# Kernel tuning notes

Hardware: AMD Instinct MI355X
Metric: run time of the kernel (lower is better)

Reference implementation:

```python
import jax, jax.numpy as jnp
import numpy as np

DIM = 384
HEADS = 8
RATES = (0.5, 0.75)  # sparse_rates
EPS = 1e-12  # torch F.normalize default eps


def _dwconv3x3(x, w):
    # depthwise 3x3, padding=1; w: [3*dim, 1, 3, 3]
    return jax.lax.conv_general_dilated(
        x, w, window_strides=(1, 1), padding=((1, 1), (1, 1)),
        feature_group_count=w.shape[0],
        dimension_numbers=('NCHW', 'OIHW', 'NCHW'))


def setup_inputs() -> dict:
    key = jax.random.key(0)
    ks = jax.random.split(key, 5)
    dim = DIM
    x = jax.random.normal(ks[0], (4, dim, 128, 128), jnp.float32)
    qkv_w = jax.random.normal(ks[1], (3 * dim, dim), jnp.float32) * 0.05   # 1x1 conv
    dw_w = jax.random.normal(ks[2], (3 * dim, 1, 3, 3), jnp.float32) * 0.1  # depthwise 3x3
    proj_w = jax.random.normal(ks[3], (dim, dim), jnp.float32) * 0.05       # 1x1 conv
    temperature = jnp.ones((HEADS, 1, 1), jnp.float32)
    attns = jnp.full((len(RATES),), 0.2, jnp.float32)
    return {"x": x, "qkv_w": qkv_w, "dw_w": dw_w, "proj_w": proj_w,
            "temperature": temperature, "attns": attns}


def reference(x, qkv_w, dw_w, proj_w, temperature, attns) -> jnp.ndarray:
    b, c, h, w = x.shape
    qkv = jnp.einsum('bchw,oc->bohw', x, qkv_w)  # 1x1 conv, no bias
    qkv = _dwconv3x3(qkv, dw_w)
    q, k, v = jnp.split(qkv, 3, axis=1)

    def heads(t):  # b (head c) h w -> b head c (h w)
        return t.reshape(b, HEADS, c // HEADS, h * w)

    q, k, v = heads(q), heads(k), heads(v)
    q = q / jnp.maximum(jnp.linalg.norm(q, axis=-1, keepdims=True), EPS)
    k = k / jnp.maximum(jnp.linalg.norm(k, axis=-1, keepdims=True), EPS)
    C = q.shape[2]
    attn = jnp.einsum('bhcn,bhdn->bhcd', q, k) * temperature  # [b, head, C, C]

    out = jnp.zeros_like(v)  # [b, head, C, HW]
    for i, rate in enumerate(RATES):
        kk = int(C * rate)
        _, idx = jax.lax.top_k(attn, kk)                      # [b, head, C, kk]
        mask = jax.nn.one_hot(idx, C, dtype=attn.dtype).sum(-2) > 0  # scatter 1s
        attn = jnp.where(mask, attn, -jnp.inf)
        attn = jax.nn.softmax(attn, axis=-1)  # NOTE: original reuses softmaxed attn next iter
        out = out + jnp.einsum('bhcd,bhdn->bhcn', attn, v) * attns[i]

    out = out.reshape(b, c, h, w)  # b head c (hw) -> b (head c) h w
    return jnp.einsum('bchw,oc->bohw', out, proj_w)
```

## Files before the change

### kernel.cpp

```cpp
#include <hip/hip_runtime.h>
#include <math.h>

#define HW     16384
#define WIDTH  128
#define CDIM   384
#define QKVC   1152
#define HEADS  8
#define CH     48
#define NSPLIT 32
#define GK     384

typedef unsigned short u16;
typedef short bf16x8 __attribute__((ext_vector_type(8)));
typedef u16 u16x8 __attribute__((ext_vector_type(8)));
typedef float f32x4 __attribute__((ext_vector_type(4)));

__device__ __forceinline__ void split2(float x, u16& h, u16& l) {
    union { float f; unsigned u; } a, b, c;
    a.f = x;
    unsigned hu = (a.u + 0x7fffu + ((a.u >> 16) & 1u)) & 0xffff0000u;
    b.u = hu;
    h = (u16)(hu >> 16);
    c.f = x - b.f;
    l = (u16)((c.u + 0x7fffu + ((c.u >> 16) & 1u)) >> 16);
}

__device__ __forceinline__ void gload16(const void* g, void* l) {
    __builtin_amdgcn_global_load_lds((const __attribute__((address_space(1))) unsigned int*)g,
                                     (__attribute__((address_space(3))) unsigned int*)l, 16, 0, 0);
}

__global__ __launch_bounds__(256)
void mfma_gemm(const u16* __restrict__ Ah, const u16* __restrict__ Al,
               const u16* __restrict__ Bh, const u16* __restrict__ Bl,
               float* __restrict__ C, int nmb,
               long abs_, long bbs, long cbs)
{
    extern __shared__ char smem[];
    const int tot = gridDim.x * gridDim.y;
    const int per = tot >> 3;
    const int fl  = blockIdx.x + gridDim.x * blockIdx.y;
    const int f2  = (fl & 7) * per + (fl >> 3);
    const int nblk = f2 / nmb, mblk = f2 % nmb;
    const int b = blockIdx.z;
    Ah += (long)b * abs_; Al += (long)b * abs_;
    Bh += (long)b * bbs;  Bl += (long)b * bbs;
    C  += (long)b * cbs;
    const int m0 = mblk * 128, n0 = nblk * 128;

    const int tid  = threadIdx.x;
    const int wave = tid >> 6, lane = tid & 63;
    const int lr = lane & 15, lg = lane >> 4;
    const int wm = wave >> 1, wn = wave & 1;

    const int srow = tid >> 2;
    const int kc   = tid & 3;
    const int sw   = kc ^ ((srow >> 1) & 3);

    f32x4 acc[4][4];
#pragma unroll
    for (int i = 0; i < 4; ++i)
#pragma unroll
        for (int j = 0; j < 4; ++j) acc[i][j] = (f32x4){0.f, 0.f, 0.f, 0.f};

#define STAGE(bs, kt) do { char* LL = smem + (bs) * 32768;                          \
        const long ko = (long)(kt) * 32 + sw * 8;                                   \
        gload16(Ah + (long)(m0 + srow) * GK      + ko, LL + tid * 16);              \
        gload16(Ah + (long)(m0 + 64 + srow) * GK + ko, LL + 4096  + tid * 16);      \
        gload16(Al + (long)(m0 + srow) * GK      + ko, LL + 8192  + tid * 16);      \
        gload16(Al + (long)(m0 + 64 + srow) * GK + ko, LL + 12288 + tid * 16);      \
        gload16(Bh + (long)(n0 + srow) * GK      + ko, LL + 16384 + tid * 16);      \
        gload16(Bh + (long)(n0 + 64 + srow) * GK + ko, LL + 20480 + tid * 16);      \
        gload16(Bl + (long)(n0 + srow) * GK      + ko, LL + 24576 + tid * 16);      \
        gload16(Bl + (long)(n0 + 64 + srow) * GK + ko, LL + 28672 + tid * 16);      \
    } while (0)

    STAGE(0, 0);
    __syncthreads();
#pragma unroll
    for (int kt = 0; kt < 12; ++kt) {
        if (kt + 1 < 12) STAGE((kt + 1) & 1, kt + 1);

        const char* L = smem + (kt & 1) * 32768;
        bf16x8 af[4][2], bf[4][2];
#pragma unroll
        for (int mi = 0; mi < 4; ++mi) {
            int r = wm * 64 + mi * 16 + lr;
            int off = r * 64 + (((lg ^ (r >> 1)) & 3) << 4);
            af[mi][0] = *(const bf16x8*)(L + off);
            af[mi][1] = *(const bf16x8*)(L + 8192 + off);
        }
#pragma unroll
        for (int ni = 0; ni < 4; ++ni) {
            int r = wn * 64 + ni * 16 + lr;
            int off = r * 64 + (((lg ^ (r >> 1)) & 3) << 4);
            bf[ni][0] = *(const bf16x8*)(L + 16384 + off);
            bf[ni][1] = *(const bf16x8*)(L + 24576 + off);
        }

        __builtin_amdgcn_s_setprio(1);
#pragma unroll
        for (int mi = 0; mi < 4; ++mi)
#pragma unroll
            for (int ni = 0; ni < 4; ++ni) {
                acc[mi][ni] = __builtin_amdgcn_mfma_f32_16x16x32_bf16(af[mi][0], bf[ni][0], acc[mi][ni], 0, 0, 0);
                acc[mi][ni] = __builtin_amdgcn_mfma_f32_16x16x32_bf16(af[mi][0], bf[ni][1], acc[mi][ni], 0, 0, 0);
                acc[mi][ni] = __builtin_amdgcn_mfma_f32_16x16x32_bf16(af[mi][1], bf[ni][0], acc[mi][ni], 0, 0, 0);
            }
        __builtin_amdgcn_s_setprio(0);
        __syncthreads();
    }
#undef STAGE

#pragma unroll
    for (int mi = 0; mi < 4; ++mi)
#pragma unroll
        for (int ni = 0; ni < 4; ++ni) {
            int row = m0 + wm * 64 + mi * 16 + lg * 4;
            int col = n0 + wn * 64 + ni * 16 + lr;
            float* cp = C + (long)row * HW + col;
            cp[0]          = acc[mi][ni][0];
            cp[(long)HW]   = acc[mi][ni][1];
            cp[2L * HW]    = acc[mi][ni][2];
            cp[3L * HW]    = acc[mi][ni][3];
        }
}

__global__ __launch_bounds__(256)
void convT_kernel(const float* __restrict__ in, u16* __restrict__ oh, u16* __restrict__ ol,
                  long ibs, long obs)
{
    const int b = blockIdx.z;
    in += (long)b * ibs; oh += (long)b * obs; ol += (long)b * obs;
    __shared__ float t[32][33];
    const int p0 = blockIdx.x * 32, c0 = blockIdx.y * 32;
    const int ty = threadIdx.x >> 5, tx = threadIdx.x & 31;
#pragma unroll
    for (int it = 0; it < 4; ++it) {
        int c = ty + it * 8;
        t[c][tx] = in[(long)(c0 + c) * HW + p0 + tx];
    }
    __syncthreads();
    const int cp = threadIdx.x & 15;
    const int py = threadIdx.x >> 4;
#pragma unroll
    for (int half = 0; half < 2; ++half) {
        int p = py + half * 16;
        u16 h0, l0, h1, l1;
        split2(t[2 * cp][p], h0, l0);
        split2(t[2 * cp + 1][p], h1, l1);
        long o = (long)(p0 + p) * CDIM + c0 + 2 * cp;
        *(ushort2*)&oh[o] = (ushort2){h0, h1};
        *(ushort2*)&ol[o] = (ushort2){l0, l1};
    }
}

__global__ __launch_bounds__(256)
void convA_kernel(const float* __restrict__ in, u16* __restrict__ oh, u16* __restrict__ ol, int n)
{
    int i = blockIdx.x * 256 + threadIdx.x;
    if (i < n) split2(in[i], oh[i], ol[i]);
}

__global__ __launch_bounds__(256)
void dwconv_kernel(const float* __restrict__ in, const float* __restrict__ w,
                   float* __restrict__ out)
{
    const long base = (long)blockIdx.y * QKVC * HW;
    const int idx = blockIdx.x * 256 + threadIdx.x;
    const int ch = idx >> 11;
    const int wi = idx & 2047;
    const int y = wi >> 4, x0 = (wi & 15) * 8;
    const float* wp = w + ch * 9;
    const float* ip = in + base + (long)ch * HW;
    float o[8] = {0.f, 0.f, 0.f, 0.f, 0.f, 0.f, 0.f, 0.f};
#pragma unroll
    for (int dy = -1; dy <= 1; ++dy) {
        int yy = y + dy;
        if ((unsigned)yy >= 128u) continue;
        const float* rp = ip + yy * WIDTH + x0;
        float4 a  = *(const float4*)rp;
        float4 bq = *(const float4*)(rp + 4);
        float v[10] = { (x0 > 0) ? rp[-1] : 0.f,
                        a.x, a.y, a.z, a.w, bq.x, bq.y, bq.z, bq.w,
                        (x0 < 120) ? rp[8] : 0.f };
        float w0 = wp[(dy + 1) * 3], w1 = wp[(dy + 1) * 3 + 1], w2 = wp[(dy + 1) * 3 + 2];
#pragma unroll
        for (int j = 0; j < 8; ++j)
            o[j] = fmaf(w0, v[j], fmaf(w1, v[j + 1], fmaf(w2, v[j + 2], o[j])));
    }
    float* op = out + base + (long)ch * HW + y * WIDTH + x0;
    *(float4*)op       = (float4){o[0], o[1], o[2], o[3]};
    *(float4*)(op + 4) = (float4){o[4], o[5], o[6], o[7]};
}

__global__ __launch_bounds__(256)
void dwconv_vT_kernel(const float* __restrict__ in, const float* __restrict__ w,
                      u16* __restrict__ oh, u16* __restrict__ ol, long ibs, long obs)
{
    const int b  = blockIdx.z;
    const int cg = blockIdx.y;
    const int p0 = blockIdx.x * 64;
    const int y  = p0 >> 7, xh = p0 & 127;
    __shared__ unsigned pk[64][97];

    const int tid = threadIdx.x;
    const int seg = tid & 7;
    const int chl = tid >> 3;
    const int x0  = xh + seg * 8;
#pragma unroll
    for (int cp = 0; cp < 3; ++cp) {
        const int cl = cp * 32 + chl;
        const int c  = cg * 96 + cl;
        const float* ip = in + (long)b * ibs + (long)(768 + c) * HW;
        const float* wp = w + (768 + c) * 9;
        float o[8] = {0.f, 0.f, 0.f, 0.f, 0.f, 0.f, 0.f, 0.f};
#pragma unroll
        for (int dy = -1; dy <= 1; ++dy) {
            int yy = y + dy;
            if ((unsigned)yy >= 128u) continue;
            const float* rp = ip + yy * WIDTH + x0;
            float4 a  = *(const float4*)rp;
            float4 bq = *(const float4*)(rp + 4);
            float v[10] = { (x0 > 0) ? rp[-1] : 0.f,
                            a.x, a.y, a.z, a.w, bq.x, bq.y, bq.z, bq.w,
                            (x0 < 120) ? rp[8] : 0.f };
            float w0 = wp[(dy + 1) * 3], w1 = wp[(dy + 1) * 3 + 1], w2 = wp[(dy + 1) * 3 + 2];
#pragma unroll
            for (int j = 0; j < 8; ++j)
                o[j] = fmaf(w0, v[j], fmaf(w1, v[j + 1], fmaf(w2, v[j + 2], o[j])));
        }
#pragma unroll
        for (int j = 0; j < 8; ++j) {
            u16 hh, ll;
            split2(o[j], hh, ll);
            pk[seg * 8 + j][cl] = ((unsigned)hh << 16) | ll;
        }
    }
    __syncthreads();
    const int px = tid >> 2, qt = tid & 3;
    u16 hs[24], ls[24];
#pragma unroll
    for (int j = 0; j < 24; ++j) {
        unsigned v = pk[px][qt * 24 + j];
        hs[j] = (u16)(v >> 16);
        ls[j] = (u16)(v & 0xffffu);
    }
    u16* ph = oh + (long)b * obs + (long)(p0 + px) * CDIM + cg * 96 + qt * 24;
    u16* pl = ol + (long)b * obs + (long)(p0 + px) * CDIM + cg * 96 + qt * 24;
#pragma unroll
    for (int j = 0; j < 3; ++j) {
        *(u16x8*)(ph + j * 8) = *(const u16x8*)&hs[j * 8];
        *(u16x8*)(pl + j * 8) = *(const u16x8*)&ls[j * 8];
    }
}

__global__ __launch_bounds__(256)
void attn_partial_kernel(const float* __restrict__ dw, float* __restrict__ part,
                         float* __restrict__ part2, long ps, long p2s)
{
    const int split = blockIdx.x, h = blockIdx.y, b = blockIdx.z;
    const int n0 = split * (HW / NSPLIT);
    const float* qbase = dw + ((long)b * QKVC + h * CH) * HW;
    const float* kbase = dw + ((long)b * QKVC + CDIM + h * CH) * HW;
    __shared__ float qs[64][49];
    __shared__ float ks[64][49];
    const int tid = threadIdx.x;
    const int tr = tid >> 4, tc = tid & 15;
    const int c0 = tr * 3, d0 = tc * 3;
    float acc[3][3] = {{0.f}};
    float qss[3] = {0.f, 0.f, 0.f}, kss[3] = {0.f, 0.f, 0.f};
    const int cA = tid >> 4;
    const int nq = (tid & 15) * 4;
    for (int ns = 0; ns < HW / NSPLIT; ns += 64) {
        __syncthreads();
#pragma unroll
        for (int t = 0; t < 3; ++t) {
            int c = cA + t * 16;
            float4 qv = *(const float4*)(qbase + (long)c * HW + n0 + ns + nq);
            float4 kv = *(const float4*)(kbase + (long)c * HW + n0 + ns + nq);
            qs[nq + 0][c] = qv.x; qs[nq + 1][c] = qv.y;
            qs[nq + 2][c] = qv.z; qs[nq + 3][c] = qv.w;
            ks[nq + 0][c] = kv.x; ks[nq + 1][c] = kv.y;
            ks[nq + 2][c] = kv.z; ks[nq + 3][c] = kv.w;
            qss[t] += qv.x * qv.x + qv.y * qv.y + qv.z * qv.z + qv.w * qv.w;
            kss[t] += kv.x * kv.x + kv.y * kv.y + kv.z * kv.z + kv.w * kv.w;
        }
        __syncthreads();
#pragma unroll 8
        for (int n = 0; n < 64; ++n) {
            float q0 = qs[n][c0], q1 = qs[n][c0 + 1], q2 = qs[n][c0 + 2];
            float k0 = ks[n][d0], k1 = ks[n][d0 + 1], k2 = ks[n][d0 + 2];
            acc[0][0] = fmaf(q0, k0, acc[0][0]); acc[0][1] = fmaf(q0, k1, acc[0][1]); acc[0][2] = fmaf(q0, k2, acc[0][2]);
            acc[1][0] = fmaf(q1, k0, acc[1][0]); acc[1][1] = fmaf(q1, k1, acc[1][1]); acc[1][2] = fmaf(q1, k2, acc[1][2]);
            acc[2][0] = fmaf(q2, k0, acc[2][0]); acc[2][1] = fmaf(q2, k1, acc[2][1]); acc[2][2] = fmaf(q2, k2, acc[2][2]);
        }
    }
#pragma unroll
    for (int m = 1; m < 16; m <<= 1) {
#pragma unroll
        for (int t = 0; t < 3; ++t) {
            qss[t] += __shfl_xor(qss[t], m);
            kss[t] += __shfl_xor(kss[t], m);
        }
    }
    if ((tid & 15) == 0) {
        float* p2 = part2 + (long)b * p2s + ((long)h * NSPLIT + split) * 96;
#pragma unroll
        for (int t = 0; t < 3; ++t) {
            p2[cA + t * 16]      = qss[t];
            p2[48 + cA + t * 16] = kss[t];
        }
    }
    float* po = part + (long)b * ps + ((long)h * NSPLIT + split) * (CH * CH);
#pragma unroll
    for (int i = 0; i < 3; ++i)
#pragma unroll
        for (int j = 0; j < 3; ++j)
            po[(c0 + i) * CH + d0 + j] = acc[i][j];
}

__global__ __launch_bounds__(256)
void attn_reduce_kernel(const float* __restrict__ part, const float* __restrict__ part2,
                        const float* __restrict__ temp, float* __restrict__ attn,
                        long ps, long p2s, long as_)
{
    const int seg = blockIdx.x, h = blockIdx.y, b = blockIdx.z;
    const float* pp = part + (long)b * ps + (long)h * NSPLIT * (CH * CH);
    const float* p2 = part2 + (long)b * p2s + (long)h * NSPLIT * 96;
    __shared__ float sinv[96];
    if (threadIdx.x < 96) {
        float s = 0.f;
        for (int sp = 0; sp < NSPLIT; ++sp) s += p2[sp * 96 + threadIdx.x];
        sinv[threadIdx.x] = 1.f / fmaxf(sqrtf(s), 1e-12f);
    }
    __syncthreads();
    const float t = temp[h];
    const int idx = seg * 256 + threadIdx.x;
    const int c = idx / CH, d = idx % CH;
    float s = 0.f;
    for (int sp = 0; sp < NSPLIT; ++sp) s += pp[sp * (CH * CH) + idx];
    attn[(long)b * as_ + (long)h * (CH * CH) + idx] = s * sinv[c] * sinv[48 + d] * t;
}

__global__ __launch_bounds__(256)
void maskw_kernel(const float* __restrict__ attn, const float* __restrict__ attns,
                  float* __restrict__ W, long as_, long ws_)
{
    const int h = blockIdx.y, b = blockIdx.z;
    const int wave = threadIdx.x >> 6, lane = threadIdx.x & 63;
    const int r = blockIdx.x * 4 + wave;
    const float* ap = attn + (long)b * as_ + (long)h * (CH * CH) + (long)r * CH;
    float a = (lane < CH) ? ap[lane] : -3.4e38f;

    int rank = 0;
#pragma unroll
    for (int j = 0; j < CH; ++j) {
        float aj = __shfl(a, j);
        rank += (aj > a) || (aj == a && j < lane);
    }
    const bool keep = (lane < CH) && (rank < 24);
    float m = keep ? a : -3.4e38f;
#pragma unroll
    for (int o = 32; o > 0; o >>= 1) m = fmaxf(m, __shfl_xor(m, o));
    float e = keep ? expf(a - m) : 0.f;
    float s = e;
#pragma unroll
    for (int o = 32; o > 0; o >>= 1) s += __shfl_xor(s, o);
    const float A1 = e / s;

    int rank2 = 0;
#pragma unroll
    for (int j = 0; j < CH; ++j) {
        float aj = __shfl(A1, j);
        rank2 += (aj > A1) || (aj == A1 && j < lane);
    }
    const bool keep2 = (lane < CH) && (rank2 < 36);
    float m2 = keep2 ? A1 : -3.4e38f;
#pragma unroll
    for (int o = 32; o > 0; o >>= 1) m2 = fmaxf(m2, __shfl_xor(m2, o));
    float e2 = keep2 ? expf(A1 - m2) : 0.f;
    float s2 = e2;
#pragma unroll
    for (int o = 32; o > 0; o >>= 1) s2 += __shfl_xor(s2, o);

    if (lane < CH)
        W[(long)b * ws_ + (long)h * (CH * CH) + (long)r * CH + lane] =
            attns[0] * A1 + attns[1] * (e2 / s2);
}

__global__ __launch_bounds__(256)
void mbuild_kernel(const float* __restrict__ P, const float* __restrict__ W,
                   u16* __restrict__ Mh, u16* __restrict__ Ml, long ws_, long ms)
{
    const int b = blockIdx.y;
    const int idx = blockIdx.x * 256 + threadIdx.x;
    const int o = idx / CDIM, col = idx % CDIM;
    const int h = col / CH, d = col % CH;
    const float* wp = W + (long)b * ws_ + (long)h * (CH * CH) + d;
    const float* pp = P + (long)o * CDIM + h * CH;
    float s = 0.f;
#pragma unroll
    for (int c = 0; c < CH; ++c) s = fmaf(pp[c], wp[c * CH], s);
    u16 hh, ll;
    split2(s, hh, ll);
    Mh[(long)b * ms + idx] = hh;
    Ml[(long)b * ms + idx] = ll;
}

extern "C" void kernel_launch(void* const* d_in, const int* in_sizes, int n_in,
                              void* d_out, int out_size, void* d_ws, size_t ws_size,
                              hipStream_t stream)
{
    const float* x      = (const float*)d_in[0];
    const float* qkv_w  = (const float*)d_in[1];
    const float* dw_w   = (const float*)d_in[2];
    const float* proj_w = (const float*)d_in[3];
    const float* temp   = (const float*)d_in[4];
    const float* attns  = (const float*)d_in[5];
    float* out = (float*)d_out;

    const size_t perbB = (size_t)QKVC * HW * 4;
    auto need = [&](int nb) -> size_t {
        return (size_t)nb * 2 * perbB + 4u * QKVC * CDIM + 4096;
    };
    int NB = 4;
    while (NB > 1 && need(NB) > ws_size) NB >>= 1;

    const long fstride = (long)(perbB / 4);
    const long ustride = (long)(perbB / 2);

    const size_t PART_B  = 27u << 20;
    const size_t PART2_B = (29u << 20) + (512u << 10);
    const size_t ATT_B   = 30u << 20;
    const size_t WM_B    = 31u << 20;
    const size_t MH_B    = 32u << 20;
    const size_t ML_B    = 33u << 20;

    char* buf1 = (char*)d_ws;
    char* buf2 = buf1 + (size_t)NB * perbB;
    u16* Ah = (u16*)(buf2 + (size_t)NB * perbB);
    u16* Al = Ah + (size_t)QKVC * CDIM;

    convA_kernel<<<dim3((QKVC * CDIM + 255) / 256), 256, 0, stream>>>(qkv_w, Ah, Al, QKVC * CDIM);

    for (int b0 = 0; b0 < 4; b0 += NB) {
        const int nb = NB;
        float* pre = (float*)buf1;
        float* dwb = (float*)buf2;
        u16* xt_h = (u16*)buf2;                u16* xt_l = xt_h + (size_t)HW * CDIM;
        u16* vt_h = (u16*)(dwb + (size_t)768 * HW);
        u16* vt_l = vt_h + (size_t)CDIM * HW;
        float* part  = (float*)(buf1 + PART_B);
        float* part2 = (float*)(buf1 + PART2_B);
        float* attn  = (float*)(buf1 + ATT_B);
        float* Wm    = (float*)(buf1 + WM_B);
        u16* Mh = (u16*)(buf1 + MH_B);
        u16* Ml = (u16*)(buf1 + ML_B);

        convT_kernel<<<dim3(HW / 32, CDIM / 32, nb), 256, 0, stream>>>(
            x + (size_t)b0 * CDIM * HW, xt_h, xt_l, (long)CDIM * HW, ustride);
        mfma_gemm<<<dim3(HW / 128, QKVC / 128, nb), 256, 65536, stream>>>(
            Ah, Al, xt_h, xt_l, pre, QKVC / 128, 0L, ustride, fstride);
        dwconv_kernel<<<dim3(768 * HW / 8 / 256, nb), 256, 0, stream>>>(pre, dw_w, dwb);
        dwconv_vT_kernel<<<dim3(HW / 64, 4, nb), 256, 0, stream>>>(pre, dw_w, vt_h, vt_l,
                                                                   fstride, ustride);
        attn_partial_kernel<<<dim3(NSPLIT, HEADS, nb), 256, 0, stream>>>(dwb, part, part2,
                                                                         fstride, fstride);
        attn_reduce_kernel<<<dim3(9, HEADS, nb), 256, 0, stream>>>(part, part2, temp, attn,
                                                                   fstride, fstride, fstride);
        maskw_kernel<<<dim3(12, HEADS, nb), 256, 0, stream>>>(attn, attns, Wm, fstride, fstride);
        mbuild_kernel<<<dim3(CDIM * CDIM / 256, nb), 256, 0, stream>>>(proj_w, Wm, Mh, Ml,
                                                                       fstride, ustride);
        mfma_gemm<<<dim3(HW / 128, CDIM / 128, nb), 256, 65536, stream>>>(
            Mh, Ml, vt_h, vt_l, out + (size_t)b0 * CDIM * HW, CDIM / 128,
            ustride, ustride, (long)CDIM * HW);
    }
}
```

Baseline: 624.1 us.

## Load GEMM A operand directly from global and transpose attn partial LDS layout

The MFMA GEMM now stages only the B operand (hi/lo) through LDS and reads the A-operand fragments straight from global memory into registers. This halves LDS use to 32 KB and sets launch bounds to allow four blocks per CU, aiming for higher occupancy. The A reads become uncoalesced per-lane 16-byte loads that go through the cache instead of LDS. Separately, attn_partial now stores Q/K tiles channel-major so both LDS writes and reads use float4 vector accesses, reducing LDS instruction count.

```diff
diff --git a/kernel.cpp b/kernel.cpp
--- a/kernel.cpp
+++ b/kernel.cpp
@@ -30,13 +30,13 @@
                                      (__attribute__((address_space(3))) unsigned int*)l, 16, 0, 0);
 }
 
-__global__ __launch_bounds__(256)
+__global__ __launch_bounds__(256, 4)
 void mfma_gemm(const u16* __restrict__ Ah, const u16* __restrict__ Al,
                const u16* __restrict__ Bh, const u16* __restrict__ Bl,
                float* __restrict__ C, int nmb,
                long abs_, long bbs, long cbs)
 {
-    extern __shared__ char smem[];
+    __shared__ char smem[32768];
     const int tot = gridDim.x * gridDim.y;
     const int per = tot >> 3;
     const int fl  = blockIdx.x + gridDim.x * blockIdx.y;
@@ -63,39 +63,35 @@
 #pragma unroll
         for (int j = 0; j < 4; ++j) acc[i][j] = (f32x4){0.f, 0.f, 0.f, 0.f};
 
-#define STAGE(bs, kt) do { char* LL = smem + (bs) * 32768;                          \
+#define STAGEB(bs, kt) do { char* LL = smem + (bs) * 16384;                         \
         const long ko = (long)(kt) * 32 + sw * 8;                                   \
-        gload16(Ah + (long)(m0 + srow) * GK      + ko, LL + tid * 16);              \
-        gload16(Ah + (long)(m0 + 64 + srow) * GK + ko, LL + 4096  + tid * 16);      \
-        gload16(Al + (long)(m0 + srow) * GK      + ko, LL + 8192  + tid * 16);      \
-        gload16(Al + (long)(m0 + 64 + srow) * GK + ko, LL + 12288 + tid * 16);      \
-        gload16(Bh + (long)(n0 + srow) * GK      + ko, LL + 16384 + tid * 16);      \
-        gload16(Bh + (long)(n0 + 64 + srow) * GK + ko, LL + 20480 + tid * 16);      \
-        gload16(Bl + (long)(n0 + srow) * GK      + ko, LL + 24576 + tid * 16);      \
-        gload16(Bl + (long)(n0 + 64 + srow) * GK + ko, LL + 28672 + tid * 16);      \
+        gload16(Bh + (long)(n0 + srow) * GK      + ko, LL + tid * 16);              \
+        gload16(Bh + (long)(n0 + 64 + srow) * GK + ko, LL + 4096  + tid * 16);      \
+        gload16(Bl + (long)(n0 + srow) * GK      + ko, LL + 8192  + tid * 16);      \
+        gload16(Bl + (long)(n0 + 64 + srow) * GK + ko, LL + 12288 + tid * 16);      \
     } while (0)
 
-    STAGE(0, 0);
+    STAGEB(0, 0);
     __syncthreads();
 #pragma unroll
     for (int kt = 0; kt < 12; ++kt) {
-        if (kt + 1 < 12) STAGE((kt + 1) & 1, kt + 1);
-
-        const char* L = smem + (kt & 1) * 32768;
-        bf16x8 af[4][2], bf[4][2];
+        bf16x8 af[4][2];
 #pragma unroll
         for (int mi = 0; mi < 4; ++mi) {
-            int r = wm * 64 + mi * 16 + lr;
-            int off = r * 64 + (((lg ^ (r >> 1)) & 3) << 4);
-            af[mi][0] = *(const bf16x8*)(L + off);
-            af[mi][1] = *(const bf16x8*)(L + 8192 + off);
-        }
+            long r = m0 + wm * 64 + mi * 16 + lr;
+            af[mi][0] = *(const bf16x8*)(Ah + r * GK + kt * 32 + lg * 8);
+            af[mi][1] = *(const bf16x8*)(Al + r * GK + kt * 32 + lg * 8);
+        }
+        if (kt + 1 < 12) STAGEB((kt + 1) & 1, kt + 1);
+
+        const char* L = smem + (kt & 1) * 16384;
+        bf16x8 bf[4][2];
 #pragma unroll
         for (int ni = 0; ni < 4; ++ni) {
             int r = wn * 64 + ni * 16 + lr;
             int off = r * 64 + (((lg ^ (r >> 1)) & 3) << 4);
-            bf[ni][0] = *(const bf16x8*)(L + 16384 + off);
-            bf[ni][1] = *(const bf16x8*)(L + 24576 + off);
+            bf[ni][0] = *(const bf16x8*)(L + off);
+            bf[ni][1] = *(const bf16x8*)(L + 8192 + off);
         }
 
         __builtin_amdgcn_s_setprio(1);
@@ -110,7 +106,7 @@
         __builtin_amdgcn_s_setprio(0);
         __syncthreads();
     }
-#undef STAGE
+#undef STAGEB
 
 #pragma unroll
     for (int mi = 0; mi < 4; ++mi)
@@ -263,8 +259,8 @@
     const int n0 = split * (HW / NSPLIT);
     const float* qbase = dw + ((long)b * QKVC + h * CH) * HW;
     const float* kbase = dw + ((long)b * QKVC + CDIM + h * CH) * HW;
-    __shared__ float qs[64][49];
-    __shared__ float ks[64][49];
+    __shared__ float qs[48][68];
+    __shared__ float ks[48][68];
     const int tid = threadIdx.x;
     const int tr = tid >> 4, tc = tid & 15;
     const int c0 = tr * 3, d0 = tc * 3;
@@ -272,6 +268,14 @@
     float qss[3] = {0.f, 0.f, 0.f}, kss[3] = {0.f, 0.f, 0.f};
     const int cA = tid >> 4;
     const int nq = (tid & 15) * 4;
+
+#define DOT4(I, J, Q, K) do {                               \
+        acc[I][J] = fmaf((Q).x, (K).x, acc[I][J]);          \
+        acc[I][J] = fmaf((Q).y, (K).y, acc[I][J]);          \
+        acc[I][J] = fmaf((Q).z, (K).z, acc[I][J]);          \
+        acc[I][J] = fmaf((Q).w, (K).w, acc[I][J]);          \
+    } while (0)
+
     for (int ns = 0; ns < HW / NSPLIT; ns += 64) {
         __syncthreads();
 #pragma unroll
@@ -279,23 +283,26 @@
             int c = cA + t * 16;
             float4 qv = *(const float4*)(qbase + (long)c * HW + n0 + ns + nq);
             float4 kv = *(const float4*)(kbase + (long)c * HW + n0 + ns + nq);
-            qs[nq + 0][c] = qv.x; qs[nq + 1][c] = qv.y;
-            qs[nq + 2][c] = qv.z; qs[nq + 3][c] = qv.w;
-            ks[nq + 0][c] = kv.x; ks[nq + 1][c] = kv.y;
-            ks[nq + 2][c] = kv.z; ks[nq + 3][c] = kv.w;
+            *(float4*)&qs[c][nq] = qv;
+            *(float4*)&ks[c][nq] = kv;
             qss[t] += qv.x * qv.x + qv.y * qv.y + qv.z * qv.z + qv.w * qv.w;
             kss[t] += kv.x * kv.x + kv.y * kv.y + kv.z * kv.z + kv.w * kv.w;
         }
         __syncthreads();
-#pragma unroll 8
-        for (int n = 0; n < 64; ++n) {
-            float q0 = qs[n][c0], q1 = qs[n][c0 + 1], q2 = qs[n][c0 + 2];
-            float k0 = ks[n][d0], k1 = ks[n][d0 + 1], k2 = ks[n][d0 + 2];
-            acc[0][0] = fmaf(q0, k0, acc[0][0]); acc[0][1] = fmaf(q0, k1, acc[0][1]); acc[0][2] = fmaf(q0, k2, acc[0][2]);
-            acc[1][0] = fmaf(q1, k0, acc[1][0]); acc[1][1] = fmaf(q1, k1, acc[1][1]); acc[1][2] = fmaf(q1, k2, acc[1][2]);
-            acc[2][0] = fmaf(q2, k0, acc[2][0]); acc[2][1] = fmaf(q2, k1, acc[2][1]); acc[2][2] = fmaf(q2, k2, acc[2][2]);
-        }
-    }
+#pragma unroll 4
+        for (int nn = 0; nn < 64; nn += 4) {
+            float4 qa = *(const float4*)&qs[c0 + 0][nn];
+            float4 qb = *(const float4*)&qs[c0 + 1][nn];
+            float4 qc = *(const float4*)&qs[c0 + 2][nn];
+            float4 ka = *(const float4*)&ks[d0 + 0][nn];
+            float4 kb = *(const float4*)&ks[d0 + 1][nn];
+            float4 kc = *(const float4*)&ks[d0 + 2][nn];
+            DOT4(0, 0, qa, ka); DOT4(0, 1, qa, kb); DOT4(0, 2, qa, kc);
+            DOT4(1, 0, qb, ka); DOT4(1, 1, qb, kb); DOT4(1, 2, qb, kc);
+            DOT4(2, 0, qc, ka); DOT4(2, 1, qc, kb); DOT4(2, 2, qc, kc);
+        }
+    }
+#undef DOT4
 #pragma unroll
     for (int m = 1; m < 16; m <<= 1) {
 #pragma unroll
@@ -460,7 +467,7 @@
 
         convT_kernel<<<dim3(HW / 32, CDIM / 32, nb), 256, 0, stream>>>(
             x + (size_t)b0 * CDIM * HW, xt_h, xt_l, (long)CDIM * HW, ustride);
-        mfma_gemm<<<dim3(HW / 128, QKVC / 128, nb), 256, 65536, stream>>>(
+        mfma_gemm<<<dim3(HW / 128, QKVC / 128, nb), 256, 0, stream>>>(
             Ah, Al, xt_h, xt_l, pre, QKVC / 128, 0L, ustride, fstride);
         dwconv_kernel<<<dim3(768 * HW / 8 / 256, nb), 256, 0, stream>>>(pre, dw_w, dwb);
         dwconv_vT_kernel<<<dim3(HW / 64, 4, nb), 256, 0, stream>>>(pre, dw_w, vt_h, vt_l,
@@ -472,7 +479,7 @@
         maskw_kernel<<<dim3(12, HEADS, nb), 256, 0, stream>>>(attn, attns, Wm, fstride, fstride);
         mbuild_kernel<<<dim3(CDIM * CDIM / 256, nb), 256, 0, stream>>>(proj_w, Wm, Mh, Ml,
                                                                        fstride, ustride);
-        mfma_gemm<<<dim3(HW / 128, CDIM / 128, nb), 256, 65536, stream>>>(
+        mfma_gemm<<<dim3(HW / 128, CDIM / 128, nb), 256, 0, stream>>>(
             Mh, Ml, vt_h, vt_l, out + (size_t)b0 * CDIM * HW, CDIM / 128,
             ustride, ustride, (long)CDIM * HW);
     }
```

Measured after the change: 1.141 ms. +82.8%, slower.
